# Optimization experiments

Hardware: AMD Instinct MI355X
Metric: run time of the kernel (lower is better)

## Reference

```python
import jax, jax.numpy as jnp
import numpy as np

C = 256
R = 16  # reduction
CR = C // R
LN_EPS = 1e-5


def setup_inputs() -> dict:
    key = jax.random.key(0)
    ks = jax.random.split(key, 8)
    B, H, W = 16, 128, 128
    x = jax.random.normal(ks[0], (B, C, H, W), dtype=jnp.float32)
    # conv_mask: Conv2d(C, 1, 1x1)
    w_mask = jax.random.normal(ks[1], (C,), dtype=jnp.float32) * (1.0 / np.sqrt(C))
    b_mask = jnp.zeros((), dtype=jnp.float32)
    # channel_add[0]: Conv2d(C, C//R, 1x1)
    w1 = jax.random.normal(ks[2], (CR, C), dtype=jnp.float32) * (1.0 / np.sqrt(C))
    b1 = jnp.zeros((CR,), dtype=jnp.float32)
    # channel_add[1]: LayerNorm([C//R, 1, 1])
    ln_g = jnp.ones((CR,), dtype=jnp.float32)
    ln_b = jnp.zeros((CR,), dtype=jnp.float32)
    # channel_add[3]: Conv2d(C//R, C, 1x1)
    w2 = jax.random.normal(ks[3], (C, CR), dtype=jnp.float32) * (1.0 / np.sqrt(CR))
    b2 = jnp.zeros((C,), dtype=jnp.float32)
    return {"x": x, "w_mask": w_mask, "b_mask": b_mask,
            "w1": w1, "b1": b1, "ln_g": ln_g, "ln_b": ln_b,
            "w2": w2, "b2": b2}


def reference(x, w_mask, b_mask, w1, b1, ln_g, ln_b, w2, b2):
    B, Cc, H, W = x.shape
    # 1x1 conv to 1 channel -> attention logits over H*W
    logits = jnp.einsum('bchw,c->bhw', x, w_mask) + b_mask          # [B,H,W]
    attn = jax.nn.softmax(logits.reshape(B, H * W), axis=-1)        # [B,HW]
    # attention-pooled global context: [B,C]
    context = jnp.einsum('bchw,bs->bc', x, attn.reshape(B, H, W).reshape(B, H * W)[:, :].reshape(B, H * W)) if False else jnp.einsum('bcs,bs->bc', x.reshape(B, Cc, H * W), attn)
    # channel_add MLP: conv1x1 -> LayerNorm over [C//R] -> ReLU -> conv1x1
    t = jnp.einsum('oc,bc->bo', w1, context) + b1                   # [B,C//R]
    mu = jnp.mean(t, axis=-1, keepdims=True)
    var = jnp.mean((t - mu) ** 2, axis=-1, keepdims=True)
    t = (t - mu) / jnp.sqrt(var + LN_EPS) * ln_g + ln_b
    t = jax.nn.relu(t)
    add = jnp.einsum('oc,bc->bo', w2, t) + b2                       # [B,C]
    return x + add[:, :, None, None]
```

## Files before the change

### kernel.cpp

```cpp
#include <hip/hip_runtime.h>
#include <math.h>

#define CC   256
#define CR   16
#define SB   16384
#define NB   16
#define ST   64
#define NT   (SB/ST)
#define LN_EPS 1e-5f

typedef float vfloat4 __attribute__((ext_vector_type(4)));

__global__ __launch_bounds__(1024) void k_ctx_partial(const float* __restrict__ x,
                                                      const float* __restrict__ w_mask,
                                                      float* __restrict__ pc,
                                                      float* __restrict__ pm,
                                                      float* __restrict__ ps) {
    __shared__ float tile[CC * ST];
    __shared__ float plog[ST * 17];
    __shared__ float pl[ST];
    __shared__ float wm[CC];
    __shared__ float red2[4 * 260];

    const int t   = threadIdx.x;
    const int bid = blockIdx.x;
    const int b   = bid / NT;
    const int s0  = (bid % NT) * ST;

    if (t < CC) wm[t] = w_mask[t];
    __syncthreads();

    {
        const int c0 = t >> 4;
        const int s4 = (t & 15) << 2;
        const float* xb = x + ((size_t)b * CC) * SB + s0 + s4;
        float4 acc = make_float4(0.f, 0.f, 0.f, 0.f);
#pragma unroll
        for (int k = 0; k < 4; ++k) {
            const int c = c0 + (k << 6);
            const float4 v = *reinterpret_cast<const float4*>(xb + (size_t)c * SB);
            *reinterpret_cast<float4*>(&tile[c * ST + s4]) = v;
            const float w = wm[c];
            acc.x += v.x * w; acc.y += v.y * w; acc.z += v.z * w; acc.w += v.w * w;
        }
        acc.x += __shfl_xor(acc.x, 16); acc.y += __shfl_xor(acc.y, 16);
        acc.z += __shfl_xor(acc.z, 16); acc.w += __shfl_xor(acc.w, 16);
        acc.x += __shfl_xor(acc.x, 32); acc.y += __shfl_xor(acc.y, 32);
        acc.z += __shfl_xor(acc.z, 32); acc.w += __shfl_xor(acc.w, 32);
        const int wv = t >> 6;
        if ((t & 63) < 16) {
            plog[(s4 + 0) * 17 + wv] = acc.x;
            plog[(s4 + 1) * 17 + wv] = acc.y;
            plog[(s4 + 2) * 17 + wv] = acc.z;
            plog[(s4 + 3) * 17 + wv] = acc.w;
        }
    }
    __syncthreads();

    if (t < ST) {
        float logit = 0.f;
#pragma unroll
        for (int i = 0; i < 16; ++i) logit += plog[t * 17 + i];
        float m = logit;
#pragma unroll
        for (int off = 32; off > 0; off >>= 1)
            m = fmaxf(m, __shfl_xor(m, off));
        const float p = __expf(logit - m);
        pl[t] = p;
        float sum = p;
#pragma unroll
        for (int off = 32; off > 0; off >>= 1)
            sum += __shfl_xor(sum, off);
        if (t == 0) { pm[bid] = m; ps[bid] = sum; }
    }
    __syncthreads();

    {
        const int c = t >> 2;
        const int q = t & 3;
        const int base = c * ST + q * 16;
        float acc2 = 0.f;
#pragma unroll
        for (int j = 0; j < 16; ++j) {
            const int idx = (j + c) & 15;
            acc2 += tile[base + idx] * pl[q * 16 + idx];
        }
        red2[q * 260 + c] = acc2;
    }
    __syncthreads();
    if (t < CC)
        pc[(size_t)bid * CC + t] = red2[t] + red2[260 + t] + red2[520 + t] + red2[780 + t];
}

__global__ __launch_bounds__(256) void k_combine_mlp(const float* __restrict__ pc,
                                                     const float* __restrict__ pm,
                                                     const float* __restrict__ ps,
                                                     const float* __restrict__ w1,
                                                     const float* __restrict__ b1,
                                                     const float* __restrict__ ln_g,
                                                     const float* __restrict__ ln_b,
                                                     const float* __restrict__ w2,
                                                     const float* __restrict__ b2,
                                                     float* __restrict__ add) {
    const int b = blockIdx.x;
    const int t = threadIdx.x;
    __shared__ float red[256];
    __shared__ float fx[NT];
    __shared__ float ctx[CC];
    __shared__ float tbuf[CR];
    __shared__ float tn[CR];

    const float m_t = pm[b * NT + t];
    red[t] = m_t; __syncthreads();
    for (int st = 128; st > 0; st >>= 1) {
        if (t < st) red[t] = fmaxf(red[t], red[t + st]);
        __syncthreads();
    }
    const float M = red[0]; __syncthreads();

    const float f = __expf(m_t - M);
    fx[t] = f;
    red[t] = ps[b * NT + t] * f; __syncthreads();
    for (int st = 128; st > 0; st >>= 1) {
        if (t < st) red[t] += red[t + st];
        __syncthreads();
    }
    const float invZ = 1.0f / red[0]; __syncthreads();

    float acc = 0.f;
#pragma unroll 4
    for (int j = 0; j < NT; ++j)
        acc += pc[((size_t)b * NT + j) * CC + t] * fx[j];
    ctx[t] = acc * invZ;
    __syncthreads();

    if (t < CR) {
        float a = b1[t];
        const float* w1r = w1 + (size_t)t * CC;
#pragma unroll 8
        for (int c = 0; c < CC; ++c) a += w1r[c] * ctx[c];
        tbuf[t] = a;
    }
    __syncthreads();
    if (t == 0) {
        float mu = 0.f;
        for (int i = 0; i < CR; ++i) mu += tbuf[i];
        mu *= (1.0f / CR);
        float var = 0.f;
        for (int i = 0; i < CR; ++i) { const float d = tbuf[i] - mu; var += d * d; }
        var *= (1.0f / CR);
        const float inv = rsqrtf(var + LN_EPS);
        for (int i = 0; i < CR; ++i) {
            const float v = (tbuf[i] - mu) * inv * ln_g[i] + ln_b[i];
            tn[i] = v > 0.f ? v : 0.f;
        }
    }
    __syncthreads();

    float a = b2[t];
    const float* w2r = w2 + (size_t)t * CR;
#pragma unroll
    for (int o = 0; o < CR; ++o) a += w2r[o] * tn[o];
    add[(size_t)b * CC + t] = a;
}

__global__ __launch_bounds__(256) void k_add(const float* __restrict__ x,
                                             const float* __restrict__ add,
                                             float* __restrict__ out) {
    const size_t idx = ((size_t)blockIdx.x * 256 + threadIdx.x) * 8;
    const size_t bc = idx / SB;
    const float a = add[bc];
    const float4 v0 = *reinterpret_cast<const float4*>(x + idx);
    const float4 v1 = *reinterpret_cast<const float4*>(x + idx + 4);
    vfloat4 o0 = {v0.x + a, v0.y + a, v0.z + a, v0.w + a};
    vfloat4 o1 = {v1.x + a, v1.y + a, v1.z + a, v1.w + a};
    __builtin_nontemporal_store(o0, reinterpret_cast<vfloat4*>(out + idx));
    __builtin_nontemporal_store(o1, reinterpret_cast<vfloat4*>(out + idx + 4));
}

extern "C" void kernel_launch(void* const* d_in, const int* in_sizes, int n_in,
                              void* d_out, int out_size, void* d_ws, size_t ws_size,
                              hipStream_t stream) {
    const float* x      = (const float*)d_in[0];
    const float* w_mask = (const float*)d_in[1];
    const float* w1     = (const float*)d_in[3];
    const float* b1     = (const float*)d_in[4];
    const float* ln_g   = (const float*)d_in[5];
    const float* ln_b   = (const float*)d_in[6];
    const float* w2     = (const float*)d_in[7];
    const float* b2     = (const float*)d_in[8];
    float* out = (float*)d_out;

    float* ws  = (float*)d_ws;
    float* pc  = ws;
    float* pm  = pc + (size_t)NB * NT * CC;
    float* ps  = pm + (size_t)NB * NT;
    float* add = ps + (size_t)NB * NT;

    k_ctx_partial<<<dim3(NB * NT), dim3(1024), 0, stream>>>(x, w_mask, pc, pm, ps);
    k_combine_mlp<<<dim3(NB), dim3(256), 0, stream>>>(pc, pm, ps, w1, b1, ln_g, ln_b, w2, b2, add);
    k_add<<<dim3(NB * CC * SB / 2048), dim3(256), 0, stream>>>(x, add, out);
}
```

Before: 176.7 us.

## Keep x tile in registers with 256-thread blocks instead of LDS tile

The context-partial kernel drops from 1024 to 256 threads per block, and each thread now holds 16 float4 values of x in registers instead of staging a 64KB tile in LDS. The weighted context sum is computed from those registers, and partial results are reduced through a smaller padded LDS buffer. This cuts LDS footprint so more blocks can be resident per CU, trading it for higher register pressure per thread.

```diff
diff --git a/kernel.cpp b/kernel.cpp
--- a/kernel.cpp
+++ b/kernel.cpp
@@ -11,56 +11,55 @@
 
 typedef float vfloat4 __attribute__((ext_vector_type(4)));
 
-__global__ __launch_bounds__(1024) void k_ctx_partial(const float* __restrict__ x,
-                                                      const float* __restrict__ w_mask,
-                                                      float* __restrict__ pc,
-                                                      float* __restrict__ pm,
-                                                      float* __restrict__ ps) {
-    __shared__ float tile[CC * ST];
-    __shared__ float plog[ST * 17];
+__global__ __launch_bounds__(256) void k_ctx_partial(const float* __restrict__ x,
+                                                     const float* __restrict__ w_mask,
+                                                     float* __restrict__ pc,
+                                                     float* __restrict__ pm,
+                                                     float* __restrict__ ps) {
+    __shared__ float plog[ST * 5];
     __shared__ float pl[ST];
     __shared__ float wm[CC];
-    __shared__ float red2[4 * 260];
+    __shared__ float red2[CC * 17];
 
     const int t   = threadIdx.x;
     const int bid = blockIdx.x;
     const int b   = bid / NT;
     const int s0  = (bid % NT) * ST;
 
-    if (t < CC) wm[t] = w_mask[t];
-    __syncthreads();
-
-    {
-        const int c0 = t >> 4;
-        const int s4 = (t & 15) << 2;
-        const float* xb = x + ((size_t)b * CC) * SB + s0 + s4;
-        float4 acc = make_float4(0.f, 0.f, 0.f, 0.f);
-#pragma unroll
-        for (int k = 0; k < 4; ++k) {
-            const int c = c0 + (k << 6);
-            const float4 v = *reinterpret_cast<const float4*>(xb + (size_t)c * SB);
-            *reinterpret_cast<float4*>(&tile[c * ST + s4]) = v;
-            const float w = wm[c];
-            acc.x += v.x * w; acc.y += v.y * w; acc.z += v.z * w; acc.w += v.w * w;
-        }
-        acc.x += __shfl_xor(acc.x, 16); acc.y += __shfl_xor(acc.y, 16);
-        acc.z += __shfl_xor(acc.z, 16); acc.w += __shfl_xor(acc.w, 16);
-        acc.x += __shfl_xor(acc.x, 32); acc.y += __shfl_xor(acc.y, 32);
-        acc.z += __shfl_xor(acc.z, 32); acc.w += __shfl_xor(acc.w, 32);
-        const int wv = t >> 6;
-        if ((t & 63) < 16) {
-            plog[(s4 + 0) * 17 + wv] = acc.x;
-            plog[(s4 + 1) * 17 + wv] = acc.y;
-            plog[(s4 + 2) * 17 + wv] = acc.z;
-            plog[(s4 + 3) * 17 + wv] = acc.w;
-        }
+    wm[t] = w_mask[t];
+    __syncthreads();
+
+    const int g  = t >> 4;
+    const int i  = t & 15;
+    const int s4 = i << 2;
+
+    const float* xb = x + (size_t)b * CC * SB + s0 + s4;
+    float4 v[16];
+    float4 acc = make_float4(0.f, 0.f, 0.f, 0.f);
+#pragma unroll
+    for (int k = 0; k < 16; ++k) {
+        const int c = g + (k << 4);
+        v[k] = *reinterpret_cast<const float4*>(xb + (size_t)c * SB);
+        const float w = wm[c];
+        acc.x += v[k].x * w; acc.y += v[k].y * w;
+        acc.z += v[k].z * w; acc.w += v[k].w * w;
+    }
+    acc.x += __shfl_xor(acc.x, 16); acc.y += __shfl_xor(acc.y, 16);
+    acc.z += __shfl_xor(acc.z, 16); acc.w += __shfl_xor(acc.w, 16);
+    acc.x += __shfl_xor(acc.x, 32); acc.y += __shfl_xor(acc.y, 32);
+    acc.z += __shfl_xor(acc.z, 32); acc.w += __shfl_xor(acc.w, 32);
+    const int wv = t >> 6;
+    if ((t & 63) < 16) {
+        plog[(s4 + 0) * 5 + wv] = acc.x;
+        plog[(s4 + 1) * 5 + wv] = acc.y;
+        plog[(s4 + 2) * 5 + wv] = acc.z;
+        plog[(s4 + 3) * 5 + wv] = acc.w;
     }
     __syncthreads();
 
     if (t < ST) {
-        float logit = 0.f;
-#pragma unroll
-        for (int i = 0; i < 16; ++i) logit += plog[t * 17 + i];
+        const float logit = plog[t * 5 + 0] + plog[t * 5 + 1]
+                          + plog[t * 5 + 2] + plog[t * 5 + 3];
         float m = logit;
 #pragma unroll
         for (int off = 32; off > 0; off >>= 1)
@@ -75,21 +74,19 @@
     }
     __syncthreads();
 
-    {
-        const int c = t >> 2;
-        const int q = t & 3;
-        const int base = c * ST + q * 16;
-        float acc2 = 0.f;
-#pragma unroll
-        for (int j = 0; j < 16; ++j) {
-            const int idx = (j + c) & 15;
-            acc2 += tile[base + idx] * pl[q * 16 + idx];
-        }
-        red2[q * 260 + c] = acc2;
-    }
-    __syncthreads();
-    if (t < CC)
-        pc[(size_t)bid * CC + t] = red2[t] + red2[260 + t] + red2[520 + t] + red2[780 + t];
+    const float p0 = pl[s4 + 0], p1 = pl[s4 + 1];
+    const float p2 = pl[s4 + 2], p3 = pl[s4 + 3];
+#pragma unroll
+    for (int k = 0; k < 16; ++k) {
+        const int c = g + (k << 4);
+        red2[c * 17 + i] = v[k].x * p0 + v[k].y * p1 + v[k].z * p2 + v[k].w * p3;
+    }
+    __syncthreads();
+
+    float s = 0.f;
+#pragma unroll
+    for (int j = 0; j < 16; ++j) s += red2[t * 17 + j];
+    pc[(size_t)bid * CC + t] = s;
 }
 
 __global__ __launch_bounds__(256) void k_combine_mlp(const float* __restrict__ pc,
@@ -197,7 +194,7 @@
     float* ps  = pm + (size_t)NB * NT;
     float* add = ps + (size_t)NB * NT;
 
-    k_ctx_partial<<<dim3(NB * NT), dim3(1024), 0, stream>>>(x, w_mask, pc, pm, ps);
+    k_ctx_partial<<<dim3(NB * NT), dim3(256), 0, stream>>>(x, w_mask, pc, pm, ps);
     k_combine_mlp<<<dim3(NB), dim3(256), 0, stream>>>(pc, pm, ps, w1, b1, ln_g, ln_b, w2, b2, add);
     k_add<<<dim3(NB * CC * SB / 2048), dim3(256), 0, stream>>>(x, add, out);
 }
```

Result: faster. 170.8 us, median of 2 (-3.3%).
